# Performance work log

Hardware: AMD Instinct MI355X
Metric: run time of the kernel (lower is better)

## Reference

```python
import jax, jax.numpy as jnp
import numpy as np
from jax import lax

B, T, N, H = 512, 128, 500, 1024
LB, UB = 0.0, 0.1
REBAL_ITERS = 20  # fixed unroll of the data-dependent while loop (converges immediately here)


def setup_inputs() -> dict:
    key = jax.random.key(0)
    ks = jax.random.split(key, 16)
    sN = 1.0 / np.sqrt(N)
    sH = 1.0 / np.sqrt(H)
    inp = {
        'x': jax.random.normal(ks[0], (B, T, N), jnp.float32),
        # GRU layer 0 (input N -> H), PyTorch gate order [r, z, n]
        'w_ih0': jax.random.normal(ks[1], (3 * H, N), jnp.float32) * sN,
        'w_hh0': jax.random.normal(ks[2], (3 * H, H), jnp.float32) * sH,
        'b_ih0': jax.random.normal(ks[3], (3 * H,), jnp.float32) * sH,
        'b_hh0': jax.random.normal(ks[4], (3 * H,), jnp.float32) * sH,
        # GRU layer 1 (H -> H)
        'w_ih1': jax.random.normal(ks[5], (3 * H, H), jnp.float32) * sH,
        'w_hh1': jax.random.normal(ks[6], (3 * H, H), jnp.float32) * sH,
        'b_ih1': jax.random.normal(ks[7], (3 * H,), jnp.float32) * sH,
        'b_hh1': jax.random.normal(ks[8], (3 * H,), jnp.float32) * sH,
        # score MLP: Linear(H,H) -> LayerNorm(H) -> SiLU -> Linear(H,N)
        'w1': jax.random.normal(ks[9], (H, H), jnp.float32) * sH,
        'b1': jax.random.normal(ks[10], (H,), jnp.float32) * sH,
        'ln_g': jnp.ones((H,), jnp.float32),
        'ln_b': jnp.zeros((H,), jnp.float32),
        'w2': jax.random.normal(ks[11], (N, H), jnp.float32) * sH,
        'b2': jax.random.normal(ks[12], (N,), jnp.float32) * sH,
    }
    return inp


def _gru_layer(x, w_ih, w_hh, b_ih, b_hh):
    # x: [B, T, D] -> hidden sequence [B, T, H]
    h_dim = w_hh.shape[1]
    x_proj = jnp.einsum('btd,gd->btg', x, w_ih) + b_ih  # [B, T, 3H]

    def step(h, xp):
        gh = jnp.einsum('bh,gh->bg', h, w_hh) + b_hh
        xr, xz, xn = jnp.split(xp, 3, axis=-1)
        hr, hz, hn = jnp.split(gh, 3, axis=-1)
        r = jax.nn.sigmoid(xr + hr)
        z = jax.nn.sigmoid(xz + hz)
        n = jnp.tanh(xn + r * hn)
        h_new = (1.0 - z) * n + z * h
        return h_new, h_new

    h0 = jnp.zeros((x.shape[0], h_dim), x.dtype)
    _, hs = lax.scan(step, h0, jnp.swapaxes(x_proj, 0, 1))  # [T, B, H]
    return jnp.swapaxes(hs, 0, 1)


def _rebalance(w, lb, ub):
    # vectorized, fixed-iteration version of the per-sample while loop
    n = w.shape[-1]
    w = jnp.clip(w, lb, ub)

    def body(w, _):
        excess = jnp.sum(w, axis=-1, keepdims=True) - 1.0
        active = excess > 1e-6
        surplus = jnp.maximum(w - ub, 0.0)
        tot_sur = jnp.sum(surplus, axis=-1, keepdims=True)
        upd = jnp.where(tot_sur > 0,
                        w - surplus / jnp.maximum(tot_sur, 1e-12) * excess,
                        w - excess / n)
        upd = jnp.clip(upd, lb, ub)
        return jnp.where(active, upd, w), None

    w, _ = lax.scan(body, w, None, length=REBAL_ITERS)
    return w


def reference(x, w_ih0, w_hh0, b_ih0, b_hh0, w_ih1, w_hh1, b_ih1, b_hh1,
              w1, b1, ln_g, ln_b, w2, b2):
    out = _gru_layer(x, w_ih0, w_hh0, b_ih0, b_hh0)
    out = _gru_layer(out, w_ih1, w_hh1, b_ih1, b_hh1)
    h_t = out[:, -1, :]  # [B, H]

    # score MLP (dropout is identity in eval)
    z = h_t @ w1.T + b1
    mu = jnp.mean(z, axis=-1, keepdims=True)
    var = jnp.var(z, axis=-1, keepdims=True)
    z = (z - mu) / jnp.sqrt(var + 1e-5) * ln_g + ln_b
    z = z * jax.nn.sigmoid(z)  # SiLU
    scores = z @ w2.T + b2  # [B, N]

    # LONG_ONLY (default True): negative scores -> -inf before softmax
    scores = jnp.where(scores < 0, -jnp.inf, scores)
    weights = jax.nn.softmax(scores, axis=-1)
    return _rebalance(weights, LB, UB)
```

## Files before the change

kernel.cpp:

```cpp
#include <hip/hip_runtime.h>
#include <math.h>

#define BATCH 512
#define SEQ_T 128
#define NIN   500
#define HID   1024
#define G3    3072

typedef float f32x4 __attribute__((ext_vector_type(4)));
typedef _Float16 half8 __attribute__((ext_vector_type(8)));

__device__ __forceinline__ void split_h2(float v, unsigned short &h, unsigned short &l) {
    _Float16 hh = (_Float16)v;
    float hf = (float)hh;
    if (fabsf(hf) < 6.103515625e-5f) { hh = (_Float16)0.f; hf = 0.f; }
    _Float16 ll = (_Float16)((v - hf) * 4096.f);
    h = __builtin_bit_cast(unsigned short, hh);
    l = __builtin_bit_cast(unsigned short, ll);
}

__device__ __forceinline__ float h2f(unsigned short u) {
    return (float)__builtin_bit_cast(_Float16, u);
}

__device__ __forceinline__ void g2lds16(const void* g, void* l) {
    __builtin_amdgcn_global_load_lds(
        (const __attribute__((address_space(1))) void*)g,
        (__attribute__((address_space(3))) void*)l,
        16, 0, 0);
}

__device__ __forceinline__ void grid_barrier(unsigned* cnt, unsigned target) {
    __syncthreads();
    if (threadIdx.x == 0) {
        __threadfence();
        __hip_atomic_fetch_add(cnt, 1u, __ATOMIC_RELAXED, __HIP_MEMORY_SCOPE_AGENT);
        while (__hip_atomic_load(cnt, __ATOMIC_RELAXED, __HIP_MEMORY_SCOPE_AGENT) < target)
            __builtin_amdgcn_s_sleep(1);
        __threadfence();
    }
    __syncthreads();
    asm volatile("" ::: "memory");
}

__global__ __launch_bounds__(512, 1) void gru_fused(
    unsigned short* __restrict__ pH, unsigned short* __restrict__ pL,
    int nslots, int mode, int tt0, int nsteps,
    const unsigned short* __restrict__ Wh, const unsigned short* __restrict__ Wl,
    const float* __restrict__ bhh,
    const float* __restrict__ gx,
    unsigned* bar)
{
    __shared__ __align__(16) unsigned short lds[3][2560 * 8];
    __shared__ float red[64][96];

    const int tid  = threadIdx.x;
    const int lane = tid & 63;
    const int wave = tid >> 6;
    const int ms = wave >> 2, ns = (wave >> 1) & 1, wk = wave & 1;
    const int q = lane >> 4, l16 = lane & 15;
    const int mt = blockIdx.x >> 5, ht = blockIdx.x & 31;
    const int bm = mt << 6, hbase = ht << 5;

    const unsigned short* wsrc[3];
    #pragma unroll
    for (int i = 0; i < 3; i++) {
        int u = tid + 512 * i;
        int pl = u / 768; int rem = u - pl * 768;
        int oct = rem / 96; int r96 = rem - oct * 96;
        int g = r96 >> 5, wr = r96 & 31;
        wsrc[i] = (pl ? Wl : Wh) + (long)((g << 10) + hbase + wr) * 1024 + oct * 8;
    }

    const int erow = tid >> 3;
    const int ecg  = (tid & 7) << 2;
    const float4 br4 = *(const float4*)&bhh[hbase + ecg];
    const float4 bz4 = *(const float4*)&bhh[1024 + hbase + ecg];
    const float4 bn4 = *(const float4*)&bhh[2048 + hbase + ecg];
    const float ks = 1.0f / 4096.0f;
    const int grow = bm + erow;
    const long po = (long)grow * 1024 + hbase + ecg;

    for (int ttl = 0; ttl < nsteps; ttl++) {
        const int step = tt0 + ttl;
        const int rs    = (mode == 0) ? ((step + nslots - 1) % nslots) : (step & 1);
        const int wslot = (mode == 0) ? (step % nslots) : ((step & 1) ^ 1);
        const unsigned short* srcH = pH + (size_t)rs * 524288;
        const unsigned short* srcL = pL + (size_t)rs * 524288;
        unsigned short* dstH = pH + (size_t)wslot * 524288;
        unsigned short* dstL = pL + (size_t)wslot * 524288;
        const float* gxt = gx + (size_t)ttl * (512 * 3072);

        const unsigned short* aH = srcH + (long)(bm + lane) * 1024 + wave * 8;
        const unsigned short* aL = srcL + (long)(bm + lane) * 1024 + wave * 8;

        const float* gp = gxt + (long)grow * 3072 + hbase + ecg;
        float4 xr = *(const float4*)gp;
        float4 xz = *(const float4*)(gp + 1024);
        float4 xn = *(const float4*)(gp + 2048);
        ushort4 hh4 = *(const ushort4*)&srcH[po];
        ushort4 hl4 = *(const ushort4*)&srcL[po];

        auto stage = [&](int b, int s) {
            const long ko = (long)s * 64;
            g2lds16(aH + ko,      &lds[b][(0 * 512 + wave * 64) * 8]);
            g2lds16(aL + ko,      &lds[b][(1 * 512 + wave * 64) * 8]);
            g2lds16(wsrc[0] + ko, &lds[b][(2 * 512 + wave * 64) * 8]);
            g2lds16(wsrc[1] + ko, &lds[b][(3 * 512 + wave * 64) * 8]);
            g2lds16(wsrc[2] + ko, &lds[b][(4 * 512 + wave * 64) * 8]);
        };

        f32x4 acc1[6] = {};
        f32x4 acc2[6] = {};
        stage(0, 0);
        stage(1, 1);
        #pragma unroll
        for (int s = 0; s < 16; s++) {
            if (s < 15)
                asm volatile("s_waitcnt vmcnt(5) lgkmcnt(0)\n\ts_barrier" ::: "memory");
            else
                asm volatile("s_waitcnt vmcnt(0) lgkmcnt(0)\n\ts_barrier" ::: "memory");
            if (s + 2 < 16) stage((s + 2) % 3, s + 2);
            const int bsel = s % 3;
            const int koq = wk * 4 + q;
            half8 ah[2], al[2], bh[3], bl[3];
            #pragma unroll
            for (int ti = 0; ti < 2; ti++) {
                int r = ms * 32 + ti * 16 + l16;
                ah[ti] = *(const half8*)&lds[bsel][(koq * 64 + r) * 8];
                al[ti] = *(const half8*)&lds[bsel][(512 + koq * 64 + r) * 8];
            }
            #pragma unroll
            for (int tj = 0; tj < 3; tj++) {
                int r = ns * 48 + tj * 16 + l16;
                bh[tj] = *(const half8*)&lds[bsel][(1024 + koq * 96 + r) * 8];
                bl[tj] = *(const half8*)&lds[bsel][(1792 + koq * 96 + r) * 8];
            }
            #pragma unroll
            for (int ti = 0; ti < 2; ti++)
            #pragma unroll
            for (int tj = 0; tj < 3; tj++) {
                int t = ti * 3 + tj;
                acc1[t] = __builtin_amdgcn_mfma_f32_16x16x32_f16(ah[ti], bh[tj], acc1[t], 0, 0, 0);
                acc2[t] = __builtin_amdgcn_mfma_f32_16x16x32_f16(ah[ti], bl[tj], acc2[t], 0, 0, 0);
                acc2[t] = __builtin_amdgcn_mfma_f32_16x16x32_f16(al[ti], bh[tj], acc2[t], 0, 0, 0);
            }
        }
        __syncthreads();
        if (wk == 1) {
            #pragma unroll
            for (int ti = 0; ti < 2; ti++)
            #pragma unroll
            for (int tj = 0; tj < 3; tj++) {
                f32x4 c = acc1[ti * 3 + tj] + acc2[ti * 3 + tj] * ks;
                #pragma unroll
                for (int rr = 0; rr < 4; rr++)
                    red[ms * 32 + ti * 16 + q * 4 + rr][ns * 48 + tj * 16 + l16] = c[rr];
            }
        }
        __syncthreads();
        if (wk == 0) {
            #pragma unroll
            for (int ti = 0; ti < 2; ti++)
            #pragma unroll
            for (int tj = 0; tj < 3; tj++) {
                f32x4 c = acc1[ti * 3 + tj] + acc2[ti * 3 + tj] * ks;
                #pragma unroll
                for (int rr = 0; rr < 4; rr++) {
                    int row = ms * 32 + ti * 16 + q * 4 + rr;
                    int col = ns * 48 + tj * 16 + l16;
                    red[row][col] += c[rr];
                }
            }
        }
        __syncthreads();
        {
            float4 sr = *(float4*)&red[erow][ecg];
            float4 sz = *(float4*)&red[erow][32 + ecg];
            float4 sn = *(float4*)&red[erow][64 + ecg];
            ushort4 oh, ol;
#define GRUC(c) { \
            float hp = h2f(hh4.c) + h2f(hl4.c) * ks; \
            float r_ = 1.f / (1.f + expf(-(xr.c + sr.c + br4.c))); \
            float z_ = 1.f / (1.f + expf(-(xz.c + sz.c + bz4.c))); \
            float n_ = tanhf(xn.c + r_ * (sn.c + bn4.c)); \
            float o_ = (1.f - z_) * n_ + z_ * hp; \
            split_h2(o_, oh.c, ol.c); }
            GRUC(x) GRUC(y) GRUC(z) GRUC(w)
#undef GRUC
            *(ushort4*)&dstH[po] = oh;
            *(ushort4*)&dstL[po] = ol;
        }
        if (ttl + 1 < nsteps)
            grid_barrier(bar, 256u * (unsigned)(ttl + 1));
    }
}

__global__ __launch_bounds__(256, 2) void gemm_h2(
    const unsigned short* __restrict__ Ah, const unsigned short* __restrict__ Al,
    const unsigned short* __restrict__ Bh, const unsigned short* __restrict__ Bl,
    const float* __restrict__ bias, float* __restrict__ C,
    int M, int NN, int Kp, int nnb)
{
    __shared__ __align__(16) unsigned short lds[2][4][8][64][8];

    const int id  = blockIdx.x;
    const int nns = nnb >> 3;
    const int xcd = id & 7;
    const int j   = id >> 3;
    const int bn  = (xcd * nns + j % nns) << 6;
    const int bm  = (j / nns) << 6;

    const int tid  = threadIdx.x;
    const int lane = tid & 63;
    const int wave = tid >> 6;
    const int ws   = wave & 1;
    const int wk   = wave >> 1;
    const int q    = lane >> 4;
    const int l16  = lane & 15;

    const unsigned short* gplane = (wave == 0) ? Ah : (wave == 1) ? Al
                                 : (wave == 2) ? Bh : Bl;
    const unsigned short* gsrc = gplane + (long)(((wave < 2) ? bm : bn) + lane) * Kp;

    f32x4 acc1[2][4] = {};
    f32x4 acc2[2][4] = {};

    const int NS = Kp >> 6;

    #pragma unroll
    for (int jk = 0; jk < 8; jk++)
        g2lds16(gsrc + jk * 8, &lds[0][wave][jk][0][0]);

    int buf = 0;
    for (int s = 0; s < NS; s++) {
        __syncthreads();
        if (s + 1 < NS) {
            const unsigned short* g2 = gsrc + (s + 1) * 64;
            #pragma unroll
            for (int jk = 0; jk < 8; jk++)
                g2lds16(g2 + jk * 8, &lds[buf ^ 1][wave][jk][0][0]);
        }
        const int ko = wk * 4 + q;
        half8 ah[2], al[2], bh[4], bl[4];
        #pragma unroll
        for (int ti = 0; ti < 2; ti++) {
            ah[ti] = *(const half8*)&lds[buf][0][ko][ws * 32 + ti * 16 + l16][0];
            al[ti] = *(const half8*)&lds[buf][1][ko][ws * 32 + ti * 16 + l16][0];
        }
        #pragma unroll
        for (int tj = 0; tj < 4; tj++) {
            bh[tj] = *(const half8*)&lds[buf][2][ko][tj * 16 + l16][0];
            bl[tj] = *(const half8*)&lds[buf][3][ko][tj * 16 + l16][0];
        }
        #pragma unroll
        for (int ti = 0; ti < 2; ti++)
        #pragma unroll
        for (int tj = 0; tj < 4; tj++) {
            acc1[ti][tj] = __builtin_amdgcn_mfma_f32_16x16x32_f16(ah[ti], bh[tj], acc1[ti][tj], 0, 0, 0);
            acc2[ti][tj] = __builtin_amdgcn_mfma_f32_16x16x32_f16(ah[ti], bl[tj], acc2[ti][tj], 0, 0, 0);
            acc2[ti][tj] = __builtin_amdgcn_mfma_f32_16x16x32_f16(al[ti], bh[tj], acc2[ti][tj], 0, 0, 0);
        }
        buf ^= 1;
    }

    __syncthreads();
    float* red = (float*)&lds[0][0][0][0][0];
    const float kscale = 1.0f / 4096.0f;
    if (wk == 1) {
        #pragma unroll
        for (int ti = 0; ti < 2; ti++)
        #pragma unroll
        for (int tj = 0; tj < 4; tj++) {
            f32x4 c = acc1[ti][tj] + acc2[ti][tj] * kscale;
            #pragma unroll
            for (int r = 0; r < 4; r++)
                red[(ws * 32 + ti * 16 + q * 4 + r) * 64 + tj * 16 + l16] = c[r];
        }
    }
    __syncthreads();
    if (wk == 0) {
        #pragma unroll
        for (int ti = 0; ti < 2; ti++)
        #pragma unroll
        for (int tj = 0; tj < 4; tj++) {
            int gn = bn + tj * 16 + l16;
            if (gn < NN) {
                float bv = bias[gn];
                f32x4 c = acc1[ti][tj] + acc2[ti][tj] * kscale;
                #pragma unroll
                for (int r = 0; r < 4; r++) {
                    int row = ws * 32 + ti * 16 + q * 4 + r;
                    C[(long)(bm + row) * NN + gn] = c[r] + red[row * 64 + tj * 16 + l16] + bv;
                }
            }
        }
    }
}

__global__ __launch_bounds__(256) void split_mat(
    const float* __restrict__ src, long outer_stride, long inner_stride, int inner_shift,
    int R, int C, int cshift,
    unsigned short* __restrict__ ph, unsigned short* __restrict__ pl)
{
    int t = blockIdx.x * 256 + threadIdx.x;
    int row = t >> cshift;
    int c0 = (t & ((1 << cshift) - 1)) << 3;
    float v[8];
    if (row < R) {
        const float* s = src + ((long)(row >> inner_shift)) * outer_stride
                             + ((long)(row & ((1 << inner_shift) - 1))) * inner_stride;
        if (c0 + 8 <= C) {
            float4 a = *(const float4*)(s + c0);
            float4 b = *(const float4*)(s + c0 + 4);
            v[0]=a.x; v[1]=a.y; v[2]=a.z; v[3]=a.w;
            v[4]=b.x; v[5]=b.y; v[6]=b.z; v[7]=b.w;
        } else {
            #pragma unroll
            for (int j2 = 0; j2 < 8; j2++) { int cc = c0 + j2; v[j2] = (cc < C) ? s[cc] : 0.f; }
        }
    } else {
        #pragma unroll
        for (int j2 = 0; j2 < 8; j2++) v[j2] = 0.f;
    }
    unsigned short hh[8], ll[8];
    #pragma unroll
    for (int j2 = 0; j2 < 8; j2++) split_h2(v[j2], hh[j2], ll[j2]);
    long o = ((long)t << 3);
    ushort4 h0 = {hh[0],hh[1],hh[2],hh[3]}, h1 = {hh[4],hh[5],hh[6],hh[7]};
    ushort4 l0 = {ll[0],ll[1],ll[2],ll[3]}, l1 = {ll[4],ll[5],ll[6],ll[7]};
    *(ushort4*)&ph[o] = h0; *(ushort4*)&ph[o + 4] = h1;
    *(ushort4*)&pl[o] = l0; *(ushort4*)&pl[o + 4] = l1;
}

__device__ __forceinline__ float block_reduce_sum(float v) {
    __shared__ float red[4];
    #pragma unroll
    for (int o = 32; o > 0; o >>= 1) v += __shfl_down(v, o);
    __syncthreads();
    if ((threadIdx.x & 63) == 0) red[threadIdx.x >> 6] = v;
    __syncthreads();
    return red[0] + red[1] + red[2] + red[3];
}

__device__ __forceinline__ float block_reduce_max(float v) {
    __shared__ float red[4];
    #pragma unroll
    for (int o = 32; o > 0; o >>= 1) v = fmaxf(v, __shfl_down(v, o));
    __syncthreads();
    if ((threadIdx.x & 63) == 0) red[threadIdx.x >> 6] = v;
    __syncthreads();
    return fmaxf(fmaxf(red[0], red[1]), fmaxf(red[2], red[3]));
}

__global__ __launch_bounds__(256) void ln_silu(
    float* __restrict__ z,
    const float* __restrict__ gamma,
    const float* __restrict__ beta,
    unsigned short* __restrict__ ph, unsigned short* __restrict__ pl)
{
    int b = blockIdx.x;
    float* row = z + (long)b * HID;
    float v[4];
    float s = 0.f;
    #pragma unroll
    for (int i = 0; i < 4; i++) { v[i] = row[threadIdx.x + 256 * i]; s += v[i]; }
    float mean = block_reduce_sum(s) * (1.f / HID);
    float vs = 0.f;
    #pragma unroll
    for (int i = 0; i < 4; i++) { float d = v[i] - mean; vs += d * d; }
    float var = block_reduce_sum(vs) * (1.f / HID);
    float inv = 1.f / sqrtf(var + 1e-5f);
    #pragma unroll
    for (int i = 0; i < 4; i++) {
        int col = threadIdx.x + 256 * i;
        float zz = (v[i] - mean) * inv * gamma[col] + beta[col];
        float sv = zz / (1.f + expf(-zz));
        row[col] = sv;
        unsigned short hh, ll;
        split_h2(sv, hh, ll);
        ph[(long)b * HID + col] = hh;
        pl[(long)b * HID + col] = ll;
    }
}

__global__ __launch_bounds__(256) void head_softmax_rebalance(
    const float* __restrict__ scores,
    float* __restrict__ out)
{
    int b = blockIdx.x;
    const float* srow = scores + (long)b * NIN;
    int i0 = threadIdx.x;
    int i1 = threadIdx.x + 256;
    bool v1 = (i1 < NIN);

    float s0 = srow[i0];
    if (s0 < 0.f) s0 = -INFINITY;
    float s1 = v1 ? srow[i1] : -INFINITY;
    if (s1 < 0.f) s1 = -INFINITY;

    float m  = block_reduce_max(fmaxf(s0, s1));
    float e0 = expf(s0 - m);
    float e1 = v1 ? expf(s1 - m) : 0.f;
    float Z  = block_reduce_sum(e0 + e1);

    float w0 = fminf(fmaxf(e0 / Z, 0.f), 0.1f);
    float w1 = v1 ? fminf(fmaxf(e1 / Z, 0.f), 0.1f) : 0.f;

    for (int it = 0; it < 20; it++) {
        float total  = block_reduce_sum(w0 + w1);
        float excess = total - 1.f;
        bool active  = excess > 1e-6f;
        float sur0 = fmaxf(w0 - 0.1f, 0.f);
        float sur1 = fmaxf(w1 - 0.1f, 0.f);
        float totsur = block_reduce_sum(sur0 + sur1);
        float u0, u1;
        if (totsur > 0.f) {
            float k = excess / fmaxf(totsur, 1e-12f);
            u0 = w0 - sur0 * k;
            u1 = w1 - sur1 * k;
        } else {
            u0 = w0 - excess / (float)NIN;
            u1 = w1 - excess / (float)NIN;
        }
        u0 = fminf(fmaxf(u0, 0.f), 0.1f);
        u1 = fminf(fmaxf(u1, 0.f), 0.1f);
        if (active) { w0 = u0; w1 = u1; }
    }

    out[(long)b * NIN + i0] = w0;
    if (v1) out[(long)b * NIN + i1] = w1;
}

extern "C" void kernel_launch(void* const* d_in, const int* in_sizes, int n_in,
                              void* d_out, int out_size, void* d_ws, size_t ws_size,
                              hipStream_t stream)
{
    const float* x     = (const float*)d_in[0];
    const float* w_ih0 = (const float*)d_in[1];
    const float* w_hh0 = (const float*)d_in[2];
    const float* b_ih0 = (const float*)d_in[3];
    const float* b_hh0 = (const float*)d_in[4];
    const float* w_ih1 = (const float*)d_in[5];
    const float* w_hh1 = (const float*)d_in[6];
    const float* b_ih1 = (const float*)d_in[7];
    const float* b_hh1 = (const float*)d_in[8];
    const float* w1    = (const float*)d_in[9];
    const float* b1    = (const float*)d_in[10];
    const float* ln_g  = (const float*)d_in[11];
    const float* ln_b  = (const float*)d_in[12];
    const float* w2    = (const float*)d_in[13];
    const float* b2    = (const float*)d_in[14];
    float* out = (float*)d_out;

    static int use_coop = -1;
    if (use_coop < 0) {
        int dev = 0; hipGetDevice(&dev);
        int ca = 0;
        hipDeviceGetAttribute(&ca, hipDeviceAttributeCooperativeLaunch, dev);
        int nb = 0;
        hipError_t e = hipOccupancyMaxActiveBlocksPerMultiprocessor(&nb, gru_fused, 512, 0);
        int ncu = 0;
        hipDeviceGetAttribute(&ncu, hipDeviceAttributeMultiprocessorCount, dev);
        use_coop = (ca && e == hipSuccess && nb >= 1 && ncu * nb >= 256) ? 1 : 0;
    }

    float* wsf = (float*)d_ws;
    auto alloc = [&](size_t nfl) { float* p = wsf; wsf += (nfl + 15) & ~(size_t)15; return p; };

    const size_t BH  = (size_t)BATCH * HID;
    const size_t BG  = (size_t)BATCH * G3;

    unsigned* bar = (unsigned*)alloc(16);
    float* zb = alloc(BH);
    float* sc = alloc((size_t)BATCH * NIN);
    unsigned short* pzbh = (unsigned short*)alloc(BH / 2);
    unsigned short* pzbl = (unsigned short*)alloc(BH / 2);
    unsigned short* ph1  = (unsigned short*)alloc(BH);
    unsigned short* pl1  = (unsigned short*)alloc(BH);
    const size_t W0 = (size_t)G3 * 512;
    const size_t WH = (size_t)G3 * HID;
    const size_t W1s = (size_t)HID * HID;
    const size_t W2s = (size_t)512 * HID;
    unsigned short* pwih0h = (unsigned short*)alloc(W0 / 2);
    unsigned short* pwih0l = (unsigned short*)alloc(W0 / 2);
    unsigned short* pwhh0h = (unsigned short*)alloc(WH / 2);
    unsigned short* pwhh0l = (unsigned short*)alloc(WH / 2);
    unsigned short* pwih1h = (unsigned short*)alloc(WH / 2);
    unsigned short* pwih1l = (unsigned short*)alloc(WH / 2);
    unsigned short* pwhh1h = (unsigned short*)alloc(WH / 2);
    unsigned short* pwhh1l = (unsigned short*)alloc(WH / 2);
    unsigned short* pw1h   = (unsigned short*)alloc(W1s / 2);
    unsigned short* pw1l   = (unsigned short*)alloc(W1s / 2);
    unsigned short* pw2h   = (unsigned short*)alloc(W2s / 2);
    unsigned short* pw2l   = (unsigned short*)alloc(W2s / 2);
    size_t fixed_floats = (size_t)(wsf - (float*)d_ws);

    int Tc = 2;
    const int cands[7] = {128, 64, 32, 16, 8, 4, 2};
    for (int ci = 0; ci < 7; ci++) {
        size_t need = fixed_floats + (size_t)cands[ci] * 2359296ULL + 4096;
        if (need * sizeof(float) <= ws_size) { Tc = cands[ci]; break; }
    }
    float* gxc = alloc((size_t)Tc * BG);
    unsigned short* pxh = (unsigned short*)alloc((size_t)Tc * BATCH * 512 / 2);
    unsigned short* pxl = (unsigned short*)alloc((size_t)Tc * BATCH * 512 / 2);
    unsigned short* ph0 = (unsigned short*)alloc((size_t)Tc * BH / 2);
    unsigned short* pl0 = (unsigned short*)alloc((size_t)Tc * BH / 2);

    hipMemsetAsync(ph0 + (size_t)(Tc - 1) * BH, 0, BH * sizeof(unsigned short), stream);
    hipMemsetAsync(pl0 + (size_t)(Tc - 1) * BH, 0, BH * sizeof(unsigned short), stream);
    hipMemsetAsync(ph1, 0, BH * sizeof(unsigned short), stream);
    hipMemsetAsync(pl1, 0, BH * sizeof(unsigned short), stream);

    dim3 blk(256);

    split_mat<<<dim3(G3 * 512 / 2048), blk, 0, stream>>>(w_ih0, 0L, (long)NIN, 30, G3, NIN, 6, pwih0h, pwih0l);
    split_mat<<<dim3(G3 * HID / 2048), blk, 0, stream>>>(w_hh0, 0L, (long)HID, 30, G3, HID, 7, pwhh0h, pwhh0l);
    split_mat<<<dim3(G3 * HID / 2048), blk, 0, stream>>>(w_ih1, 0L, (long)HID, 30, G3, HID, 7, pwih1h, pwih1l);
    split_mat<<<dim3(G3 * HID / 2048), blk, 0, stream>>>(w_hh1, 0L, (long)HID, 30, G3, HID, 7, pwhh1h, pwhh1l);
    split_mat<<<dim3(HID * HID / 2048), blk, 0, stream>>>(w1, 0L, (long)HID, 30, HID, HID, 7, pw1h, pw1l);
    split_mat<<<dim3(512 * HID / 2048), blk, 0, stream>>>(w2, 0L, (long)HID, 30, NIN, HID, 7, pw2h, pw2l);

    auto launch_gru = [&](unsigned short* pHb, unsigned short* pLb, int nslots, int mode,
                          int tt0, int nsteps,
                          const unsigned short* Whp, const unsigned short* Wlp,
                          const float* bhhp, const float* gxp) {
        if (use_coop) {
            hipMemsetAsync(bar, 0, sizeof(unsigned), stream);
            void* args[] = {&pHb, &pLb, &nslots, &mode, &tt0, &nsteps,
                            (void*)&Whp, (void*)&Wlp, (void*)&bhhp, (void*)&gxp,
                            (void*)&bar};
            hipLaunchCooperativeKernel(gru_fused, dim3(256), dim3(512), args, 0, stream);
        } else {
            for (int tt = 0; tt < nsteps; tt++)
                gru_fused<<<dim3(256), dim3(512), 0, stream>>>(
                    pHb, pLb, nslots, mode, tt0 + tt, 1, Whp, Wlp, bhhp,
                    gxp + (size_t)tt * (512 * 3072), bar);
        }
    };

    for (int c = 0; c < SEQ_T / Tc; c++) {
        int t0 = c * Tc;
        split_mat<<<dim3(Tc * BATCH * 512 / 2048), blk, 0, stream>>>(
            x + (long)t0 * NIN, (long)NIN, (long)SEQ_T * NIN, 9,
            Tc * BATCH, NIN, 6, pxh, pxl);
        gemm_h2<<<dim3((Tc * BATCH / 64) * 48), blk, 0, stream>>>(
            pxh, pxl, pwih0h, pwih0l, b_ih0, gxc, Tc * BATCH, G3, 512, 48);
        launch_gru(ph0, pl0, Tc, 0, 0, Tc, pwhh0h, pwhh0l, b_hh0, gxc);
        gemm_h2<<<dim3((Tc * BATCH / 64) * 48), blk, 0, stream>>>(
            ph0, pl0, pwih1h, pwih1l, b_ih1, gxc, Tc * BATCH, G3, 1024, 48);
        launch_gru(ph1, pl1, 2, 1, t0, Tc, pwhh1h, pwhh1l, b_hh1, gxc);
    }
    gemm_h2<<<dim3(8 * 16), blk, 0, stream>>>(ph1, pl1, pw1h, pw1l, b1, zb, BATCH, HID, 1024, 16);
    ln_silu<<<dim3(BATCH), blk, 0, stream>>>(zb, ln_g, ln_b, pzbh, pzbl);
    gemm_h2<<<dim3(8 * 8), blk, 0, stream>>>(pzbh, pzbl, pw2h, pw2l, b2, sc, BATCH, NIN, 1024, 8);
    head_softmax_rebalance<<<dim3(BATCH), blk, 0, stream>>>(sc, out);
}
```

Baseline: 14.59 ms.

## Deepen GRU staging pipeline, lighten grid barrier, and launch persistent kernel without cooperative API

The fused GRU kernel now runs a 4-buffer LDS ring with three stages in flight instead of three buffers with two. The reduction scratch reuses the staging buffer so the extra buffer fits in LDS. The grid barrier uses release/acquire atomics instead of full threadfences, and the barrier counter is reset once and advanced through a running base instead of a memset before each launch. On devices with at least 256 CUs the kernel is launched normally rather than cooperatively, which removes cooperative-launch overhead but relies on all 256 blocks being co-resident.

```diff
diff --git a/kernel.cpp b/kernel.cpp
--- a/kernel.cpp
+++ b/kernel.cpp
@@ -33,11 +33,10 @@
 __device__ __forceinline__ void grid_barrier(unsigned* cnt, unsigned target) {
     __syncthreads();
     if (threadIdx.x == 0) {
-        __threadfence();
-        __hip_atomic_fetch_add(cnt, 1u, __ATOMIC_RELAXED, __HIP_MEMORY_SCOPE_AGENT);
+        __hip_atomic_fetch_add(cnt, 1u, __ATOMIC_RELEASE, __HIP_MEMORY_SCOPE_AGENT);
         while (__hip_atomic_load(cnt, __ATOMIC_RELAXED, __HIP_MEMORY_SCOPE_AGENT) < target)
-            __builtin_amdgcn_s_sleep(1);
-        __threadfence();
+            __builtin_amdgcn_s_sleep(2);
+        (void)__hip_atomic_load(cnt, __ATOMIC_ACQUIRE, __HIP_MEMORY_SCOPE_AGENT);
     }
     __syncthreads();
     asm volatile("" ::: "memory");
@@ -49,10 +48,9 @@
     const unsigned short* __restrict__ Wh, const unsigned short* __restrict__ Wl,
     const float* __restrict__ bhh,
     const float* __restrict__ gx,
-    unsigned* bar)
+    unsigned* bar, unsigned tbase)
 {
-    __shared__ __align__(16) unsigned short lds[3][2560 * 8];
-    __shared__ float red[64][96];
+    __shared__ __align__(16) unsigned short lds[4][2560 * 8];
 
     const int tid  = threadIdx.x;
     const int lane = tid & 63;
@@ -114,14 +112,17 @@
         f32x4 acc2[6] = {};
         stage(0, 0);
         stage(1, 1);
+        stage(2, 2);
         #pragma unroll
         for (int s = 0; s < 16; s++) {
-            if (s < 15)
+            if (s <= 13)
+                asm volatile("s_waitcnt vmcnt(10) lgkmcnt(0)\n\ts_barrier" ::: "memory");
+            else if (s == 14)
                 asm volatile("s_waitcnt vmcnt(5) lgkmcnt(0)\n\ts_barrier" ::: "memory");
             else
                 asm volatile("s_waitcnt vmcnt(0) lgkmcnt(0)\n\ts_barrier" ::: "memory");
-            if (s + 2 < 16) stage((s + 2) % 3, s + 2);
-            const int bsel = s % 3;
+            if (s + 3 < 16) stage((s + 3) & 3, s + 3);
+            const int bsel = s & 3;
             const int koq = wk * 4 + q;
             half8 ah[2], al[2], bh[3], bl[3];
             #pragma unroll
@@ -147,6 +148,7 @@
             }
         }
         __syncthreads();
+        float (*red)[96] = reinterpret_cast<float (*)[96]>(&lds[0][0]);
         if (wk == 1) {
             #pragma unroll
             for (int ti = 0; ti < 2; ti++)
@@ -192,7 +194,7 @@
             *(ushort4*)&dstL[po] = ol;
         }
         if (ttl + 1 < nsteps)
-            grid_barrier(bar, 256u * (unsigned)(ttl + 1));
+            grid_barrier(bar, tbase + 256u * (unsigned)(ttl + 1));
     }
 }
 
@@ -453,16 +455,16 @@
     const float* b2    = (const float*)d_in[14];
     float* out = (float*)d_out;
 
-    static int use_coop = -1;
-    if (use_coop < 0) {
+    static int launch_mode = -1;
+    if (launch_mode < 0) {
         int dev = 0; hipGetDevice(&dev);
+        int ncu = 0;
+        hipDeviceGetAttribute(&ncu, hipDeviceAttributeMultiprocessorCount, dev);
         int ca = 0;
         hipDeviceGetAttribute(&ca, hipDeviceAttributeCooperativeLaunch, dev);
-        int nb = 0;
-        hipError_t e = hipOccupancyMaxActiveBlocksPerMultiprocessor(&nb, gru_fused, 512, 0);
-        int ncu = 0;
-        hipDeviceGetAttribute(&ncu, hipDeviceAttributeMultiprocessorCount, dev);
-        use_coop = (ca && e == hipSuccess && nb >= 1 && ncu * nb >= 256) ? 1 : 0;
+        if (ncu >= 256) launch_mode = 2;
+        else if (ca)    launch_mode = 1;
+        else            launch_mode = 0;
     }
 
     float* wsf = (float*)d_ws;
@@ -508,6 +510,7 @@
     unsigned short* ph0 = (unsigned short*)alloc((size_t)Tc * BH / 2);
     unsigned short* pl0 = (unsigned short*)alloc((size_t)Tc * BH / 2);
 
+    hipMemsetAsync(bar, 0, sizeof(unsigned), stream);
     hipMemsetAsync(ph0 + (size_t)(Tc - 1) * BH, 0, BH * sizeof(unsigned short), stream);
     hipMemsetAsync(pl0 + (size_t)(Tc - 1) * BH, 0, BH * sizeof(unsigned short), stream);
     hipMemsetAsync(ph1, 0, BH * sizeof(unsigned short), stream);
@@ -522,21 +525,27 @@
     split_mat<<<dim3(HID * HID / 2048), blk, 0, stream>>>(w1, 0L, (long)HID, 30, HID, HID, 7, pw1h, pw1l);
     split_mat<<<dim3(512 * HID / 2048), blk, 0, stream>>>(w2, 0L, (long)HID, 30, NIN, HID, 7, pw2h, pw2l);
 
+    unsigned tbase = 0;
+
     auto launch_gru = [&](unsigned short* pHb, unsigned short* pLb, int nslots, int mode,
                           int tt0, int nsteps,
                           const unsigned short* Whp, const unsigned short* Wlp,
                           const float* bhhp, const float* gxp) {
-        if (use_coop) {
-            hipMemsetAsync(bar, 0, sizeof(unsigned), stream);
+        if (launch_mode == 2) {
+            gru_fused<<<dim3(256), dim3(512), 0, stream>>>(
+                pHb, pLb, nslots, mode, tt0, nsteps, Whp, Wlp, bhhp, gxp, bar, tbase);
+            tbase += 256u * (unsigned)(nsteps - 1);
+        } else if (launch_mode == 1) {
             void* args[] = {&pHb, &pLb, &nslots, &mode, &tt0, &nsteps,
                             (void*)&Whp, (void*)&Wlp, (void*)&bhhp, (void*)&gxp,
-                            (void*)&bar};
+                            (void*)&bar, &tbase};
             hipLaunchCooperativeKernel(gru_fused, dim3(256), dim3(512), args, 0, stream);
+            tbase += 256u * (unsigned)(nsteps - 1);
         } else {
             for (int tt = 0; tt < nsteps; tt++)
                 gru_fused<<<dim3(256), dim3(512), 0, stream>>>(
                     pHb, pLb, nslots, mode, tt0 + tt, 1, Whp, Wlp, bhhp,
-                    gxp + (size_t)tt * (512 * 3072), bar);
+                    gxp + (size_t)tt * (512 * 3072), bar, 0u);
         }
     };
 
```

Result: slower. 16.92 ms (+16.0%).
